# Performance work log

Hardware: AMD Instinct MI355X
Metric: run time of the kernel (lower is better)

Reference implementation:

```python
import jax, jax.numpy as jnp
import numpy as np

SPATIAL_SHAPES = np.array([[100, 100], [50, 50], [25, 25], [13, 13]], dtype=np.int32)
EMBED, NH, NL, NP = 256, 8, 4, 4
HD = EMBED // NH  # 32


def setup_inputs() -> dict:
    key = jax.random.key(0)
    ks = jax.random.split(key, 12)
    bs, nq = 4, 4000
    nv = int((SPATIAL_SHAPES[:, 0] * SPATIAL_SHAPES[:, 1]).sum())  # 13294
    s_lin = 1.0 / np.sqrt(EMBED)  # xavier-ish scale
    s_small = 0.02                # offsets/weights heads start near init
    return {
        "query": jax.random.normal(ks[0], (bs, nq, EMBED), jnp.float32),
        "value": jax.random.normal(ks[1], (bs, nv, EMBED), jnp.float32),
        "reference_points": jax.random.uniform(ks[2], (bs, nq, NL, 2), jnp.float32),
        "spatial_shapes": jnp.asarray(SPATIAL_SHAPES),
        "W_off": jax.random.normal(ks[3], (EMBED, NH * NL * NP * 2), jnp.float32) * s_small,
        "b_off": jax.random.normal(ks[4], (NH * NL * NP * 2,), jnp.float32) * s_small,
        "W_attn": jax.random.normal(ks[5], (EMBED, NH * NL * NP), jnp.float32) * s_small,
        "b_attn": jax.random.normal(ks[6], (NH * NL * NP,), jnp.float32) * s_small,
        "W_val": jax.random.normal(ks[7], (EMBED, EMBED), jnp.float32) * s_lin,
        "b_val": jnp.zeros((EMBED,), jnp.float32),
        "W_out": jax.random.normal(ks[8], (EMBED, EMBED), jnp.float32) * s_lin,
        "b_out": jnp.zeros((EMBED,), jnp.float32),
    }


def _bilinear_sample(val_l, H, W, x, y):
    """grid_sample(mode=bilinear, padding=zeros, align_corners=False) equivalent.
    val_l: [bs, nh, H*W, hd]; x, y: [bs, nh, nq, np] pixel-space coords.
    Returns [bs, nh, nq, np, hd]."""
    x0 = jnp.floor(x)
    y0 = jnp.floor(y)
    bs, nh, nq, npts = x.shape
    out = 0.0
    for dx, dy in ((0, 0), (1, 0), (0, 1), (1, 1)):
        xi = x0 + dx
        yi = y0 + dy
        w = (1.0 - jnp.abs(x - xi)) * (1.0 - jnp.abs(y - yi))
        valid = (xi >= 0) & (xi < W) & (yi >= 0) & (yi < H)
        idx = (jnp.clip(yi, 0, H - 1) * W + jnp.clip(xi, 0, W - 1)).astype(jnp.int32)
        g = jnp.take_along_axis(val_l, idx.reshape(bs, nh, nq * npts, 1), axis=2)
        g = g.reshape(bs, nh, nq, npts, -1)
        out = out + g * (w * valid.astype(w.dtype))[..., None]
    return out


def reference(query, value, reference_points, spatial_shapes,
              W_off, b_off, W_attn, b_attn, W_val, b_val, W_out, b_out):
    shapes = np.asarray(spatial_shapes)  # static level shapes
    bs, nq, _ = query.shape
    # value projection -> per-head layout [bs, nh, nv, hd]
    v = (value @ W_val + b_val).reshape(bs, -1, NH, HD).transpose(0, 2, 1, 3)
    # sampling offsets and attention weights from query
    off = (query @ W_off + b_off).reshape(bs, nq, NH, NL, NP, 2)
    attn = jax.nn.softmax((query @ W_attn + b_attn).reshape(bs, nq, NH, NL * NP), axis=-1)
    attn = attn.reshape(bs, nq, NH, NL, NP)
    # normalized sampling locations; normalizer = (W, H) per level
    normalizer = jnp.asarray(np.stack([shapes[:, 1], shapes[:, 0]], -1), jnp.float32)
    loc = reference_points[:, :, None, :, None, :] + off / normalizer[None, None, None, :, None, :]
    out = jnp.zeros((bs, NH, nq, HD), query.dtype)
    start = 0
    for l in range(NL):
        H, W = int(shapes[l, 0]), int(shapes[l, 1])
        val_l = v[:, :, start:start + H * W, :]
        # pixel coords with align_corners=False: p = loc*size - 0.5
        x = loc[:, :, :, l, :, 0].transpose(0, 2, 1, 3) * W - 0.5  # [bs,nh,nq,np]
        y = loc[:, :, :, l, :, 1].transpose(0, 2, 1, 3) * H - 0.5
        sampled = _bilinear_sample(val_l, H, W, x, y)  # [bs,nh,nq,np,hd]
        out = out + jnp.einsum('bhqpd,bqhp->bhqd', sampled, attn[:, :, :, l, :])
        start += H * W
    out = out.transpose(0, 2, 1, 3).reshape(bs, nq, EMBED)
    return out @ W_out + b_out
```

## Files before the change

### kernel.cpp

```cpp
#include <hip/hip_runtime.h>
#include <hip/hip_bf16.h>

#define EMBED 256
#define NH 8
#define NL 4
#define NP 4
#define HD 32
#define BS 4
#define NQ 4000
#define NV 13294

using f32x4   = __attribute__((ext_vector_type(4))) float;
using bf16x8  = __attribute__((ext_vector_type(8))) short;

__device__ __forceinline__ float bf2f_lo(unsigned u) {
    union { unsigned u; float f; } x; x.u = u << 16; return x.f;
}
__device__ __forceinline__ float bf2f_hi(unsigned u) {
    union { unsigned u; float f; } x; x.u = u & 0xffff0000u; return x.f;
}
__device__ __forceinline__ unsigned short f2bf(float f) {
    union { float f; unsigned u; } x; x.f = f;
    unsigned u = x.u;
    return (unsigned short)((u + 0x7fffu + ((u >> 16) & 1u)) >> 16);
}
__device__ __forceinline__ unsigned cvtpk(float lo, float hi) {
    unsigned r;
    asm("v_cvt_pk_bf16_f32 %0, %1, %2" : "=v"(r) : "v"(lo), "v"(hi));
    return r;
}

__device__ __forceinline__ void async16(const void* g, void* l) {
    __builtin_amdgcn_global_load_lds(
        (const __attribute__((address_space(1))) void*)g,
        (__attribute__((address_space(3))) void*)l, 16, 0, 0);
}

template<int N> __device__ __forceinline__ void wait_vmcnt() {
    if constexpr (N == 0)      asm volatile("s_waitcnt vmcnt(0)" ::: "memory");
    else if constexpr (N == 3) asm volatile("s_waitcnt vmcnt(3)" ::: "memory");
    else if constexpr (N == 4) asm volatile("s_waitcnt vmcnt(4)" ::: "memory");
}

__global__ __launch_bounds__(256) void msda_prep_k(
    const float* __restrict__ W_val, const float* __restrict__ W_out,
    const float* __restrict__ W_off, const float* __restrict__ W_attn,
    const float* __restrict__ b_off, const float* __restrict__ b_attn,
    unsigned short* __restrict__ Wt_val, unsigned short* __restrict__ Wt_out,
    unsigned short* __restrict__ Wt_qa, float* __restrict__ b_qa)
{
    int i = blockIdx.x * 256 + threadIdx.x;
    if (i < 384) b_qa[i] = (i < 256) ? b_off[i] : b_attn[i - 256];
    if (i < 65536) {
        int r = i >> 8, c = i & 255;
        Wt_val[c * 256 + r] = f2bf(W_val[i]);
    } else if (i < 131072) {
        int j = i - 65536, r = j >> 8, c = j & 255;
        Wt_out[c * 256 + r] = f2bf(W_out[j]);
    } else if (i < 229376) {
        int j = i - 131072;
        int n = j >> 8, k = j & 255;
        float v = (n < 256) ? W_off[k * 256 + n] : W_attn[k * 128 + (n - 256)];
        Wt_qa[j] = f2bf(v);
    }
}

template<int TM, int EPI, bool ABF16>
__device__ __forceinline__ void gemm_body(
    char* lds,
    const void* __restrict__ Ap,
    const unsigned short* __restrict__ Bt,
    const float* __restrict__ bias,
    void* __restrict__ out,
    int M, int N, int mblk, int nblk)
{
    constexpr int K = 256, C = 8;
    constexpr int NI = 2;
    constexpr int ABYTES = TM * 32 * (ABF16 ? 2 : 4);
    constexpr int BBYTES = 128 * 32 * 2;
    constexpr int BUFB = ABYTES + BBYTES;
    constexpr int AIPW = ABYTES / 4096;
    constexpr int DPW  = AIPW + 2;

    const int m0 = mblk * TM, n0 = nblk * 128;
    const int tid  = threadIdx.x;
    const int w    = tid >> 6;
    const int lane = tid & 63;
    const int quad = lane >> 4;
    const int l16  = lane & 15;
    const int wn   = w * 32;

    const char* agp[AIPW];
#pragma unroll
    for (int j = 0; j < AIPW; j++) {
        int ai = w * AIPW + j;
        if constexpr (ABF16) {
            int row  = ai * 16 + (lane >> 2);
            int rowg = min(m0 + row, M - 1);
            int scol = (lane & 3) ^ ((lane >> 2) & 3);
            agp[j] = (const char*)Ap + (size_t)rowg * 512 + scol * 16;
        } else {
            int row  = ai * 8 + (lane >> 3);
            int rowg = min(m0 + row, M - 1);
            int scol = (lane & 7) ^ (lane >> 3);
            agp[j] = (const char*)Ap + (size_t)rowg * 1024 + scol * 16;
        }
    }
    const char* bgp[2];
#pragma unroll
    for (int j = 0; j < 2; j++) {
        int bi   = w * 2 + j;
        int row  = bi * 16 + (lane >> 2);
        int scol = (lane & 3) ^ ((lane >> 2) & 3);
        bgp[j] = (const char*)Bt + (size_t)(n0 + row) * 512 + scol * 16;
    }

    auto issue = [&](int c, int kb) {
        char* aL = lds + kb * BUFB;
        char* bL = aL + ABYTES;
        const int ko = c * (ABF16 ? 64 : 128);
#pragma unroll
        for (int j = 0; j < AIPW; j++)
            async16(agp[j] + ko, aL + (w * AIPW + j) * 1024);
#pragma unroll
        for (int j = 0; j < 2; j++)
            async16(bgp[j] + c * 64, bL + (w * 2 + j) * 1024);
    };

    f32x4 acc[4][NI];
#pragma unroll
    for (int a = 0; a < 4; a++)
#pragma unroll
        for (int b = 0; b < NI; b++) acc[a][b] = (f32x4){0.f, 0.f, 0.f, 0.f};

    issue(0, 0);
    issue(1, 1);
#pragma unroll
    for (int c = 0; c < C; c++) {
        if (c + 1 < C) wait_vmcnt<DPW>(); else wait_vmcnt<0>();
        __builtin_amdgcn_s_barrier();
        __builtin_amdgcn_sched_barrier(0);
        if (c + 2 < C) issue(c + 2, (c + 2) % 3);

        const char* aL = lds + (c % 3) * BUFB;
        const char* bL = aL + ABYTES;
        bf16x8 af[4], bfr[NI];
#pragma unroll
        for (int mi = 0; mi < 4; mi++) {
            int row = mi * 16 + l16;
            if constexpr (ABF16) {
                af[mi] = *(const bf16x8*)(aL + row * 64 + ((quad ^ (row & 3)) * 16));
            } else {
                f32x4 lo = *(const f32x4*)(aL + row * 128 + (((2 * quad)     ^ (row & 7)) * 16));
                f32x4 hi = *(const f32x4*)(aL + row * 128 + (((2 * quad + 1) ^ (row & 7)) * 16));
                union { unsigned u[4]; bf16x8 v; } t;
                t.u[0] = cvtpk(lo[0], lo[1]); t.u[1] = cvtpk(lo[2], lo[3]);
                t.u[2] = cvtpk(hi[0], hi[1]); t.u[3] = cvtpk(hi[2], hi[3]);
                af[mi] = t.v;
            }
        }
#pragma unroll
        for (int ni = 0; ni < NI; ni++) {
            int row = wn + ni * 16 + l16;
            bfr[ni] = *(const bf16x8*)(bL + row * 64 + ((quad ^ (row & 3)) * 16));
        }
#pragma unroll
        for (int mi = 0; mi < 4; mi++)
#pragma unroll
            for (int ni = 0; ni < NI; ni++)
                acc[mi][ni] = __builtin_amdgcn_mfma_f32_16x16x32_bf16(af[mi], bfr[ni], acc[mi][ni], 0, 0, 0);
    }

    if constexpr (EPI == 0) {
        __syncthreads();
        unsigned short* cs = (unsigned short*)lds;
#pragma unroll
        for (int ni = 0; ni < NI; ni++) {
            int cl = wn + ni * 16 + l16;
            float bvv = bias[n0 + cl];
#pragma unroll
            for (int mi = 0; mi < 4; mi++)
#pragma unroll
                for (int r = 0; r < 4; r++) {
                    int ml = mi * 16 + quad * 4 + r;
                    cs[ml * 136 + cl] = f2bf(acc[mi][ni][r] + bvv);
                }
        }
        __syncthreads();
        const int row = tid >> 2, seg = tid & 3;
        const int m = m0 + row;
        if (m < M) {
            const uint4* s = (const uint4*)&cs[row * 136 + seg * 32];
            uint4* d = (uint4*)((unsigned short*)out + (size_t)m * N + n0 + seg * 32);
#pragma unroll
            for (int j = 0; j < 4; j++) d[j] = s[j];
        }
    } else {
#pragma unroll
        for (int ni = 0; ni < NI; ni++) {
            int cc = n0 + wn + ni * 16 + l16;
            float bvv = bias[cc];
#pragma unroll
            for (int mi = 0; mi < 4; mi++)
#pragma unroll
                for (int r = 0; r < 4; r++) {
                    int m = m0 + mi * 16 + quad * 4 + r;
                    if (m >= M) continue;
                    ((float*)out)[(size_t)m * N + cc] = acc[mi][ni][r] + bvv;
                }
        }
    }
}

__global__ __launch_bounds__(256) void msda_gemm_vq_k(
    const float* __restrict__ value, const float* __restrict__ query,
    const unsigned short* __restrict__ Wt_val, const unsigned short* __restrict__ Wt_qa,
    const float* __restrict__ b_val, const float* __restrict__ b_qa,
    unsigned short* __restrict__ v_buf, float* __restrict__ oa_buf)
{
    extern __shared__ char lds[];
    const int bx = blockIdx.x;
    if (bx < 1662) {
        gemm_body<64, 0, false>(lds, value, Wt_val, b_val, v_buf,
                                BS * NV, 256, bx >> 1, bx & 1);
    } else {
        const int j = bx - 1662;
        const int mb = j / 3;
        gemm_body<64, 1, false>(lds, query, Wt_qa, b_qa, oa_buf,
                                BS * NQ, 384, mb, j - mb * 3);
    }
}

__global__ __launch_bounds__(256) void msda_gemm_out_k(
    const unsigned short* __restrict__ t_buf,
    const unsigned short* __restrict__ Wt_out,
    const float* __restrict__ b_out,
    float* __restrict__ out)
{
    extern __shared__ char lds[];
    const int bx = blockIdx.x;
    gemm_body<64, 1, true>(lds, t_buf, Wt_out, b_out, out,
                           BS * NQ, 256, bx >> 1, bx & 1);
}

__global__ __launch_bounds__(256) void msda_sampler_k(
    const float* __restrict__ refpts,
    const float* __restrict__ oa_buf,
    const unsigned short* __restrict__ v_buf,
    unsigned short* __restrict__ t_out)
{
    __shared__ float  oa_s[4][384];
    __shared__ float  ref_s[4][8];
    __shared__ float4 wtab[528];
    __shared__ int4   itab[528];

    const int tid = threadIdx.x;
    const int q0  = blockIdx.x * 4;

    {
        const float4* src = (const float4*)(oa_buf + (size_t)q0 * 384);
        float4* dst = (float4*)&oa_s[0][0];
        dst[tid] = src[tid];
        if (tid < 128) dst[256 + tid] = src[256 + tid];
        if (tid < 32) ((float*)ref_s)[tid] = refpts[q0 * 8 + tid];
    }
    __syncthreads();

    const int HWs[4]    = {100, 50, 25, 13};
    const int starts[4] = {0, 10000, 12500, 13125};
#pragma unroll
    for (int it = 0; it < 2; it++) {
        int s  = tid + it * 256;
        int i  = s & 15;
        int h  = (s >> 4) & 7;
        int ql = s >> 7;
        int l  = i >> 2, p = i & 3;
        float logit = oa_s[ql][256 + h * 16 + i];
        float m = logit;
#pragma unroll
        for (int off = 1; off < 16; off <<= 1) m = fmaxf(m, __shfl_xor(m, off, 64));
        float e = __expf(logit - m);
        float sum = e;
#pragma unroll
        for (int off = 1; off < 16; off <<= 1) sum += __shfl_xor(sum, off, 64);
        float a = e / sum;

        int Wl = HWs[l];
        float fW = (float)Wl;
        float rx = ref_s[ql][l * 2], ry = ref_s[ql][l * 2 + 1];
        float offx = oa_s[ql][h * 32 + l * 8 + p * 2];
        float offy = oa_s[ql][h * 32 + l * 8 + p * 2 + 1];
        float x = rx * fW + offx - 0.5f;
        float y = ry * fW + offy - 0.5f;
        float xf = floorf(x), yf = floorf(y);
        float fx = x - xf, fy = y - yf;
        int x0 = (int)xf, y0 = (int)yf;
        int x1 = x0 + 1, y1 = y0 + 1;
        float wx0 = (x0 >= 0 && x0 < Wl) ? (1.f - fx) : 0.f;
        float wx1 = (x1 >= 0 && x1 < Wl) ? fx : 0.f;
        float wy0 = (y0 >= 0 && y0 < Wl) ? (1.f - fy) : 0.f;
        float wy1 = (y1 >= 0 && y1 < Wl) ? fy : 0.f;
        int x0c = min(max(x0, 0), Wl - 1), x1c = min(max(x1, 0), Wl - 1);
        int y0c = min(max(y0, 0), Wl - 1), y1c = min(max(y1, 0), Wl - 1);
        int r0 = starts[l] + y0c * Wl, r1 = starts[l] + y1c * Wl;
        int ti = i * 33 + ql * 8 + h;
        wtab[ti] = make_float4(wx0 * wy0 * a, wx1 * wy0 * a, wx0 * wy1 * a, wx1 * wy1 * a);
        itab[ti] = make_int4(r0 + x0c, r0 + x1c, r1 + x0c, r1 + x1c);
    }
    __syncthreads();

    const int dg = tid & 7, h = (tid >> 3) & 7, ql = tid >> 6;
    const int q = q0 + ql;
    const int b = q / NQ;
    const char* base = (const char*)v_buf + (size_t)b * NV * 512;
    const unsigned hd8 = (unsigned)h * 64 + (unsigned)dg * 8;
    const int tbase = ql * 8 + h;

    float a0 = 0.f, a1 = 0.f, a2 = 0.f, a3 = 0.f;
#pragma unroll
    for (int lp = 0; lp < 16; lp++) {
        float4 wv = wtab[lp * 33 + tbase];
        int4   ix = itab[lp * 33 + tbase];
        uint2 s0 = *(const uint2*)(base + (((unsigned)ix.x << 9) + hd8));
        uint2 s1 = *(const uint2*)(base + (((unsigned)ix.y << 9) + hd8));
        uint2 s2 = *(const uint2*)(base + (((unsigned)ix.z << 9) + hd8));
        uint2 s3 = *(const uint2*)(base + (((unsigned)ix.w << 9) + hd8));
        a0 += wv.x * bf2f_lo(s0.x); a1 += wv.x * bf2f_hi(s0.x);
        a2 += wv.x * bf2f_lo(s0.y); a3 += wv.x * bf2f_hi(s0.y);
        a0 += wv.y * bf2f_lo(s1.x); a1 += wv.y * bf2f_hi(s1.x);
        a2 += wv.y * bf2f_lo(s1.y); a3 += wv.y * bf2f_hi(s1.y);
        a0 += wv.z * bf2f_lo(s2.x); a1 += wv.z * bf2f_hi(s2.x);
        a2 += wv.z * bf2f_lo(s2.y); a3 += wv.z * bf2f_hi(s2.y);
        a0 += wv.w * bf2f_lo(s3.x); a1 += wv.w * bf2f_hi(s3.x);
        a2 += wv.w * bf2f_lo(s3.y); a3 += wv.w * bf2f_hi(s3.y);
    }
    unsigned o0 = (unsigned)f2bf(a0) | ((unsigned)f2bf(a1) << 16);
    unsigned o1 = (unsigned)f2bf(a2) | ((unsigned)f2bf(a3) << 16);
    uint2 o = {o0, o1};
    *(uint2*)(t_out + (size_t)q * 256 + h * 32 + dg * 4) = o;
}

extern "C" void kernel_launch(void* const* d_in, const int* in_sizes, int n_in,
                              void* d_out, int out_size, void* d_ws, size_t ws_size,
                              hipStream_t stream) {
    const float* query  = (const float*)d_in[0];
    const float* value  = (const float*)d_in[1];
    const float* refpts = (const float*)d_in[2];
    const float* W_off  = (const float*)d_in[4];
    const float* b_off  = (const float*)d_in[5];
    const float* W_attn = (const float*)d_in[6];
    const float* b_attn = (const float*)d_in[7];
    const float* W_val  = (const float*)d_in[8];
    const float* b_val  = (const float*)d_in[9];
    const float* W_out  = (const float*)d_in[10];
    const float* b_out  = (const float*)d_in[11];

    char* wsp = (char*)d_ws;
    size_t o = 0;
    auto carve = [&](size_t bytes) -> void* {
        void* p = wsp + o; o += (bytes + 255) & ~(size_t)255; return p;
    };
    unsigned short* Wt_val = (unsigned short*)carve(256 * 256 * 2);
    unsigned short* Wt_out = (unsigned short*)carve(256 * 256 * 2);
    unsigned short* Wt_qa  = (unsigned short*)carve(384 * 256 * 2);
    float*          b_qa   = (float*)carve(384 * 4);
    unsigned short* v_buf  = (unsigned short*)carve((size_t)BS * NV * EMBED * 2);
    float*          oa_buf = (float*)carve((size_t)BS * NQ * 384 * 4);
    unsigned short* t_buf  = (unsigned short*)carve((size_t)BS * NQ * EMBED * 2);

    msda_prep_k<<<896, 256, 0, stream>>>(W_val, W_out, W_off, W_attn,
                                         b_off, b_attn, Wt_val, Wt_out, Wt_qa, b_qa);

    msda_gemm_vq_k<<<1662 + 750, 256, 49152, stream>>>(value, query, Wt_val, Wt_qa,
                                                       b_val, b_qa, v_buf, oa_buf);
    msda_sampler_k<<<(BS * NQ) / 4, 256, 0, stream>>>(refpts, oa_buf, v_buf, t_buf);
    msda_gemm_out_k<<<500, 256, 36864, stream>>>(t_buf, Wt_out, b_out, (float*)d_out);
}
```

Baseline: 196.1 us.

## Convert A tiles to bf16 in registers and store value projection head-major

The GEMM A operand is now loaded from global memory into registers, converted to bf16 there, and written to LDS as bf16 one stage ahead. The previous path async-copied fp32 into LDS. This halves the A footprint in LDS and drops the vq kernel's shared memory from 48 KB to 36 KB, which may allow more blocks per CU. The value projection output is now written head-major ([b][h][pix][32]), so each sampler gather reads a compact 64-byte row per head, which should improve cache-line locality. The trade-off is more register pressure, direct global loads in place of async copies, and unswizzled LDS reads that may cause bank conflicts.

Result: no change. 196.0 us (-0.0%).

```diff
diff --git a/kernel.cpp b/kernel.cpp
--- a/kernel.cpp
+++ b/kernel.cpp
@@ -65,7 +65,7 @@
     }
 }
 
-template<int TM, int EPI, bool ABF16>
+template<int EPI, bool ABF16>
 __device__ __forceinline__ void gemm_body(
     char* lds,
     const void* __restrict__ Ap,
@@ -76,13 +76,12 @@
 {
     constexpr int K = 256, C = 8;
     constexpr int NI = 2;
-    constexpr int ABYTES = TM * 32 * (ABF16 ? 2 : 4);
+    constexpr int ABYTES = 64 * 32 * 2;
     constexpr int BBYTES = 128 * 32 * 2;
-    constexpr int BUFB = ABYTES + BBYTES;
-    constexpr int AIPW = ABYTES / 4096;
-    constexpr int DPW  = AIPW + 2;
-
-    const int m0 = mblk * TM, n0 = nblk * 128;
+    constexpr int BUFB   = ABYTES + BBYTES;
+    constexpr int LOPS   = ABF16 ? 1 : 2;
+
+    const int m0 = mblk * 64, n0 = nblk * 128;
     const int tid  = threadIdx.x;
     const int w    = tid >> 6;
     const int lane = tid & 63;
@@ -90,42 +89,45 @@
     const int l16  = lane & 15;
     const int wn   = w * 32;
 
-    const char* agp[AIPW];
-#pragma unroll
-    for (int j = 0; j < AIPW; j++) {
-        int ai = w * AIPW + j;
+    const int ar  = w * 16 + (lane >> 2);
+    const int arg = min(m0 + ar, M - 1);
+    const int ak  = (lane & 3) * 8;
+    const float*          afp = (const float*)Ap          + (size_t)arg * K + ak;
+    const unsigned short* abp = (const unsigned short*)Ap + (size_t)arg * K + ak;
+
+    const int brseg = lane >> 2, bcb = (lane & 3) * 16;
+    const char* bgp0 = (const char*)(Bt + (size_t)(n0 + (2 * w) * 16 + brseg) * K) + bcb;
+    const char* bgp1 = (const char*)(Bt + (size_t)(n0 + (2 * w + 1) * 16 + brseg) * K) + bcb;
+
+    auto issueB = [&](int c, int kb) {
+        char* bL = lds + kb * BUFB + ABYTES;
+        async16(bgp0 + c * 64, bL + (2 * w) * 1024);
+        async16(bgp1 + c * 64, bL + (2 * w + 1) * 1024);
+    };
+
+    float4 aLoR[2], aHiR[2];
+    bf16x8 aRegR[2];
+    auto loadA = [&](int c) {
+        const int p = c & 1;
         if constexpr (ABF16) {
-            int row  = ai * 16 + (lane >> 2);
-            int rowg = min(m0 + row, M - 1);
-            int scol = (lane & 3) ^ ((lane >> 2) & 3);
-            agp[j] = (const char*)Ap + (size_t)rowg * 512 + scol * 16;
+            aRegR[p] = *(const bf16x8*)(abp + c * 32);
         } else {
-            int row  = ai * 8 + (lane >> 3);
-            int rowg = min(m0 + row, M - 1);
-            int scol = (lane & 7) ^ (lane >> 3);
-            agp[j] = (const char*)Ap + (size_t)rowg * 1024 + scol * 16;
-        }
-    }
-    const char* bgp[2];
-#pragma unroll
-    for (int j = 0; j < 2; j++) {
-        int bi   = w * 2 + j;
-        int row  = bi * 16 + (lane >> 2);
-        int scol = (lane & 3) ^ ((lane >> 2) & 3);
-        bgp[j] = (const char*)Bt + (size_t)(n0 + row) * 512 + scol * 16;
-    }
-
-    auto issue = [&](int c, int kb) {
-        char* aL = lds + kb * BUFB;
-        char* bL = aL + ABYTES;
-        const int ko = c * (ABF16 ? 64 : 128);
-#pragma unroll
-        for (int j = 0; j < AIPW; j++)
-            async16(agp[j] + ko, aL + (w * AIPW + j) * 1024);
-#pragma unroll
-        for (int j = 0; j < 2; j++)
-            async16(bgp[j] + c * 64, bL + (w * 2 + j) * 1024);
+            aLoR[p] = *(const float4*)(afp + c * 32);
+            aHiR[p] = *(const float4*)(afp + c * 32 + 4);
+        }
     };
+    auto writeA = [&](int c) {
+        const int p = c & 1;
+        unsigned short* dst = (unsigned short*)(lds + (c % 3) * BUFB) + ar * 32 + ak;
+        if constexpr (ABF16) {
+            *(bf16x8*)dst = aRegR[p];
+        } else {
+            union { unsigned u[4]; bf16x8 v; } t;
+            t.u[0] = cvtpk(aLoR[p].x, aLoR[p].y); t.u[1] = cvtpk(aLoR[p].z, aLoR[p].w);
+            t.u[2] = cvtpk(aHiR[p].x, aHiR[p].y); t.u[3] = cvtpk(aHiR[p].z, aHiR[p].w);
+            *(bf16x8*)dst = t.v;
+        }
+    };
 
     f32x4 acc[4][NI];
 #pragma unroll
@@ -133,37 +135,29 @@
 #pragma unroll
         for (int b = 0; b < NI; b++) acc[a][b] = (f32x4){0.f, 0.f, 0.f, 0.f};
 
-    issue(0, 0);
-    issue(1, 1);
+    loadA(0); issueB(0, 0); loadA(1); issueB(1, 1);
+    writeA(0);
+
 #pragma unroll
     for (int c = 0; c < C; c++) {
-        if (c + 1 < C) wait_vmcnt<DPW>(); else wait_vmcnt<0>();
+        if (c < C - 1) wait_vmcnt<LOPS + 2>(); else wait_vmcnt<0>();
+        asm volatile("s_waitcnt lgkmcnt(0)" ::: "memory");
         __builtin_amdgcn_s_barrier();
         __builtin_amdgcn_sched_barrier(0);
-        if (c + 2 < C) issue(c + 2, (c + 2) % 3);
+        if (c + 2 < C) { loadA(c + 2); issueB(c + 2, (c + 2) % 3); }
 
         const char* aL = lds + (c % 3) * BUFB;
         const char* bL = aL + ABYTES;
         bf16x8 af[4], bfr[NI];
 #pragma unroll
-        for (int mi = 0; mi < 4; mi++) {
-            int row = mi * 16 + l16;
-            if constexpr (ABF16) {
-                af[mi] = *(const bf16x8*)(aL + row * 64 + ((quad ^ (row & 3)) * 16));
-            } else {
-                f32x4 lo = *(const f32x4*)(aL + row * 128 + (((2 * quad)     ^ (row & 7)) * 16));
-                f32x4 hi = *(const f32x4*)(aL + row * 128 + (((2 * quad + 1) ^ (row & 7)) * 16));
-                union { unsigned u[4]; bf16x8 v; } t;
-                t.u[0] = cvtpk(lo[0], lo[1]); t.u[1] = cvtpk(lo[2], lo[3]);
-                t.u[2] = cvtpk(hi[0], hi[1]); t.u[3] = cvtpk(hi[2], hi[3]);
-                af[mi] = t.v;
-            }
-        }
-#pragma unroll
-        for (int ni = 0; ni < NI; ni++) {
-            int row = wn + ni * 16 + l16;
-            bfr[ni] = *(const bf16x8*)(bL + row * 64 + ((quad ^ (row & 3)) * 16));
-        }
+        for (int mi = 0; mi < 4; mi++)
+            af[mi] = *(const bf16x8*)(aL + (mi * 16 + l16) * 64 + quad * 16);
+#pragma unroll
+        for (int ni = 0; ni < NI; ni++)
+            bfr[ni] = *(const bf16x8*)(bL + (wn + ni * 16 + l16) * 64 + quad * 16);
+
+        if (c + 1 < C) writeA(c + 1);
+
 #pragma unroll
         for (int mi = 0; mi < 4; mi++)
 #pragma unroll
@@ -187,13 +181,18 @@
                 }
         }
         __syncthreads();
-        const int row = tid >> 2, seg = tid & 3;
-        const int m = m0 + row;
+        const int rr = w * 16 + (lane >> 2);
+        const int jj = lane & 3;
+        const int m  = m0 + rr;
         if (m < M) {
-            const uint4* s = (const uint4*)&cs[row * 136 + seg * 32];
-            uint4* d = (uint4*)((unsigned short*)out + (size_t)m * N + n0 + seg * 32);
-#pragma unroll
-            for (int j = 0; j < 4; j++) d[j] = s[j];
+            const int b   = m / NV;
+            const int pix = m - b * NV;
+#pragma unroll
+            for (int seg = 0; seg < 4; seg++) {
+                const int h = (n0 >> 5) + seg;
+                uint4 s = *(const uint4*)&cs[rr * 136 + seg * 32 + jj * 8];
+                *(uint4*)((char*)out + (((size_t)b * 8 + h) * NV + pix) * 64 + jj * 16) = s;
+            }
         }
     } else {
 #pragma unroll
@@ -221,13 +220,13 @@
     extern __shared__ char lds[];
     const int bx = blockIdx.x;
     if (bx < 1662) {
-        gemm_body<64, 0, false>(lds, value, Wt_val, b_val, v_buf,
-                                BS * NV, 256, bx >> 1, bx & 1);
+        gemm_body<0, false>(lds, value, Wt_val, b_val, v_buf,
+                            BS * NV, 256, bx >> 1, bx & 1);
     } else {
         const int j = bx - 1662;
         const int mb = j / 3;
-        gemm_body<64, 1, false>(lds, query, Wt_qa, b_qa, oa_buf,
-                                BS * NQ, 384, mb, j - mb * 3);
+        gemm_body<1, false>(lds, query, Wt_qa, b_qa, oa_buf,
+                            BS * NQ, 384, mb, j - mb * 3);
     }
 }
 
@@ -239,8 +238,8 @@
 {
     extern __shared__ char lds[];
     const int bx = blockIdx.x;
-    gemm_body<64, 1, true>(lds, t_buf, Wt_out, b_out, out,
-                           BS * NQ, 256, bx >> 1, bx & 1);
+    gemm_body<1, true>(lds, t_buf, Wt_out, b_out, out,
+                       BS * NQ, 256, bx >> 1, bx & 1);
 }
 
 __global__ __launch_bounds__(256) void msda_sampler_k(
@@ -312,8 +311,7 @@
     const int dg = tid & 7, h = (tid >> 3) & 7, ql = tid >> 6;
     const int q = q0 + ql;
     const int b = q / NQ;
-    const char* base = (const char*)v_buf + (size_t)b * NV * 512;
-    const unsigned hd8 = (unsigned)h * 64 + (unsigned)dg * 8;
+    const char* base = (const char*)v_buf + ((size_t)(b * 8 + h)) * NV * 64 + dg * 8;
     const int tbase = ql * 8 + h;
 
     float a0 = 0.f, a1 = 0.f, a2 = 0.f, a3 = 0.f;
@@ -321,10 +319,10 @@
     for (int lp = 0; lp < 16; lp++) {
         float4 wv = wtab[lp * 33 + tbase];
         int4   ix = itab[lp * 33 + tbase];
-        uint2 s0 = *(const uint2*)(base + (((unsigned)ix.x << 9) + hd8));
-        uint2 s1 = *(const uint2*)(base + (((unsigned)ix.y << 9) + hd8));
-        uint2 s2 = *(const uint2*)(base + (((unsigned)ix.z << 9) + hd8));
-        uint2 s3 = *(const uint2*)(base + (((unsigned)ix.w << 9) + hd8));
+        uint2 s0 = *(const uint2*)(base + ((unsigned)ix.x << 6));
+        uint2 s1 = *(const uint2*)(base + ((unsigned)ix.y << 6));
+        uint2 s2 = *(const uint2*)(base + ((unsigned)ix.z << 6));
+        uint2 s3 = *(const uint2*)(base + ((unsigned)ix.w << 6));
         a0 += wv.x * bf2f_lo(s0.x); a1 += wv.x * bf2f_hi(s0.x);
         a2 += wv.x * bf2f_lo(s0.y); a3 += wv.x * bf2f_hi(s0.y);
         a0 += wv.y * bf2f_lo(s1.x); a1 += wv.y * bf2f_hi(s1.x);
@@ -364,14 +362,14 @@
     unsigned short* Wt_out = (unsigned short*)carve(256 * 256 * 2);
     unsigned short* Wt_qa  = (unsigned short*)carve(384 * 256 * 2);
     float*          b_qa   = (float*)carve(384 * 4);
-    unsigned short* v_buf  = (unsigned short*)carve((size_t)BS * NV * EMBED * 2);
+    unsigned short* v_buf  = (unsigned short*)carve((size_t)BS * NH * NV * 32 * 2);
     float*          oa_buf = (float*)carve((size_t)BS * NQ * 384 * 4);
     unsigned short* t_buf  = (unsigned short*)carve((size_t)BS * NQ * EMBED * 2);
 
     msda_prep_k<<<896, 256, 0, stream>>>(W_val, W_out, W_off, W_attn,
                                          b_off, b_attn, Wt_val, Wt_out, Wt_qa, b_qa);
 
-    msda_gemm_vq_k<<<1662 + 750, 256, 49152, stream>>>(value, query, Wt_val, Wt_qa,
+    msda_gemm_vq_k<<<1662 + 750, 256, 36864, stream>>>(value, query, Wt_val, Wt_qa,
                                                        b_val, b_qa, v_buf, oa_buf);
     msda_sampler_k<<<(BS * NQ) / 4, 256, 0, stream>>>(refpts, oa_buf, v_buf, t_buf);
     msda_gemm_out_k<<<500, 256, 36864, stream>>>(t_buf, Wt_out, b_out, (float*)d_out);
```
